# Kernel optimization log

Hardware: AMD Instinct MI355X
Metric: run time of the kernel (lower is better)

## Reference

```python
import jax, jax.numpy as jnp
import numpy as np

T, B, COV, H, L = 512, 256, 128, 512, 2
N_DIST_PARAMS = 2  # lnormal


def setup_inputs() -> dict:
    key = jax.random.key(0)
    ks = jax.random.split(key, 20)
    d = {}
    d["x"] = jax.random.normal(ks[0], (T, B, COV + 1), jnp.float32)
    lengths = jax.random.randint(ks[1], (B,), 2, T + 1)
    lengths = -jnp.sort(-lengths)  # packed sequences: descending lengths
    lengths = lengths.at[0].set(T)  # ensure max length == T
    d["lengths"] = lengths
    d["h0"] = jax.random.normal(ks[2], (L, B, H), jnp.float32)
    s = 1.0 / np.sqrt(H)
    in_dims = [COV + 1, H]
    for l in range(L):
        d[f"Wih{l}"] = jax.random.uniform(ks[3 + 4 * l], (3 * H, in_dims[l]), jnp.float32, -s, s)
        d[f"Whh{l}"] = jax.random.uniform(ks[4 + 4 * l], (3 * H, H), jnp.float32, -s, s)
        d[f"bih{l}"] = jax.random.uniform(ks[5 + 4 * l], (3 * H,), jnp.float32, -s, s)
        d[f"bhh{l}"] = jax.random.uniform(ks[6 + 4 * l], (3 * H,), jnp.float32, -s, s)
    sc = 1.0 / np.sqrt(H + 1)
    d["W_cov"] = jax.random.uniform(ks[11], (COV, H + 1), jnp.float32, -sc, sc)
    d["b_cov"] = jax.random.uniform(ks[12], (COV,), jnp.float32, -sc, sc)
    sp = 1.0 / np.sqrt(L * H)
    d["W_par"] = jax.random.uniform(ks[13], (N_DIST_PARAMS, L * H), jnp.float32, -sp, sp)
    d["b_par"] = jax.random.uniform(ks[14], (N_DIST_PARAMS,), jnp.float32, -sp, sp)
    return d


def gru_layer(x, h0, lengths, Wih, Whh, bih, bhh):
    # x: [T, B, D]; h0: [B, H]. PyTorch GRU gate math, masked for ragged lengths
    gi = jnp.einsum('tbd,gd->tbg', x, Wih) + bih  # [T, B, 3H], one big GEMM
    tt = jnp.arange(x.shape[0])

    def step(h, inp):
        gi_t, t = inp
        gh = h @ Whh.T + bhh
        i_r, i_z, i_n = jnp.split(gi_t, 3, axis=-1)
        h_r, h_z, h_n = jnp.split(gh, 3, axis=-1)
        r = jax.nn.sigmoid(i_r + h_r)
        z = jax.nn.sigmoid(i_z + h_z)
        n = jnp.tanh(i_n + r * h_n)
        h_new = (1.0 - z) * n + z * h
        valid = (t < lengths)[:, None]
        h = jnp.where(valid, h_new, h)          # freeze carry past length
        out = jnp.where(valid, h_new, 0.0)       # pad_packed_sequence zero-pads
        return h, out

    h_last, outs = jax.lax.scan(step, h0, (gi, tt))
    return outs, h_last


def reference(x, lengths, h0, Wih0, Whh0, bih0, bhh0, Wih1, Whh1, bih1, bhh1, W_cov, b_cov, W_par, b_par):
    o0, hl0 = gru_layer(x, h0[0], lengths, Wih0, Whh0, bih0, bhh0)
    o1, hl1 = gru_layer(o0, h0[1], lengths, Wih1, Whh1, bih1, bhh1)
    hs = jnp.transpose(o1, (1, 0, 2))  # [B, T, H]
    times = x[:, :, 0].T               # [B, T]
    hwt = jnp.concatenate([hs, times[..., None]], axis=-1)  # [B, T, H+1]
    Tm = x.shape[0]
    # batched masked matmul replacing per-(batch, timestep) GEMV loop
    preds = jnp.einsum('bth,ch->btc', hwt[:, :Tm - 1], W_cov) + b_cov  # [B, T-1, COV]
    mask = (jnp.arange(Tm - 1)[None, :] < (lengths - 1)[:, None])[..., None]
    preds = jnp.where(mask, preds, 0.0)
    # original writes COV values into a COV+1 wide zero buffer; last channel stays 0
    preds = jnp.concatenate([preds, jnp.zeros(preds.shape[:2] + (1,), preds.dtype)], axis=-1)
    last_hidden = jnp.stack([hl0, hl1])                      # [L, B, H]
    last_flat = jnp.reshape(last_hidden, (last_hidden.shape[1], -1))  # torch .view semantics
    dist_params = last_flat @ W_par.T + b_par
    return preds, jnp.exp(-dist_params)
```

## Files before the change

kernel.cpp:

```cpp
#include <hip/hip_runtime.h>


typedef unsigned short u16;
typedef unsigned long long u64;
typedef __attribute__((ext_vector_type(8))) short short8;
typedef short8 bf16x8;
typedef __attribute__((ext_vector_type(4))) float f32x4;

#define T_DIM 512
#define B_DIM 256
#define H_DIM 512
#define G3H   1536
#define BT    131072
#define XPK   192
#define PRED_ELEMS 16875264
#define SENT  0x7FC0u

#define GLD16(gp, lp) __builtin_amdgcn_global_load_lds( \
    (const __attribute__((address_space(1))) void*)(gp), \
    (__attribute__((address_space(3))) void*)(lp), 16, 0, 0)

__device__ __forceinline__ u16 f2bf(float f) {
    union { float f; unsigned i; } v; v.f = f;
    unsigned i = v.i;
    return (u16)((i + 0x7FFFu + ((i >> 16) & 1u)) >> 16);
}
__device__ __forceinline__ float bf2f(u16 u) {
    union { unsigned i; float f; } v; v.i = ((unsigned)u) << 16; return v.f;
}
__device__ __forceinline__ float sigm(float x) { return 1.f / (1.f + __expf(-x)); }
__device__ __forceinline__ float tanh_f(float x) {
    float ax = fabsf(x);
    float e = __expf(-2.f * ax);
    float t = (1.f - e) / (1.f + e);
    return x < 0.f ? -t : t;
}
__device__ __forceinline__ bf16x8 aload16(const u16* p) {
    union { bf16x8 v; u64 q[2]; } r;
    const u64* qp = (const u64*)p;
    r.q[0] = __hip_atomic_load(qp + 0, __ATOMIC_RELAXED, __HIP_MEMORY_SCOPE_AGENT);
    r.q[1] = __hip_atomic_load(qp + 1, __ATOMIC_RELAXED, __HIP_MEMORY_SCOPE_AGENT);
    return r.v;
}
__device__ __forceinline__ unsigned chk8(bf16x8 v) {
    union { bf16x8 v; unsigned d[4]; } u; u.v = v;
    unsigned b = 0;
#pragma unroll
    for (int i = 0; i < 4; ++i) {
        unsigned d = u.d[i] ^ 0x7FC07FC0u;
        b |= (unsigned)((d & 0xFFFFu) == 0u) | (unsigned)((d >> 16) == 0u);
    }
    return b;
}

__global__ void prep_kernel(const float* __restrict__ Wih0, const float* __restrict__ Wih1,
                            const float* __restrict__ Whh0, const float* __restrict__ Whh1,
                            const float* __restrict__ h0,   const float* __restrict__ Wcov,
                            u16* __restrict__ wih0b, u16* __restrict__ wih1b,
                            u16* __restrict__ whh0b, u16* __restrict__ whh1b,
                            u16* __restrict__ h0bf,  u16* __restrict__ wcovb,
                            float* __restrict__ wlastf,
                            u16* __restrict__ o0c, u16* __restrict__ o1c, int TC) {
    const int gid = blockIdx.x * 256 + threadIdx.x;
    const int gsz = gridDim.x * 256;
    for (int i = gid; i < 128; i += gsz) wlastf[i] = Wcov[i * 513 + 512];
    for (int i = gid; i < 128 * 512; i += gsz) {
        int r = i >> 9, c = i & 511;
        wcovb[i] = f2bf(Wcov[r * 513 + c]);
    }
    for (int i = gid; i < 512 * 512; i += gsz) h0bf[i] = f2bf(h0[i]);
    for (int i = gid; i < 1536 * 192; i += gsz) {
        int r = i / 192, c = i - r * 192;
        wih0b[i] = f2bf(c < 129 ? Wih0[r * 129 + c] : 0.f);
    }
    for (int i = gid; i < 1536 * 512; i += gsz) wih1b[i] = f2bf(Wih1[i]);
    for (int i = gid; i < 1536 * 512; i += gsz) whh0b[i] = f2bf(Whh0[i]);
    for (int i = gid; i < 1536 * 512; i += gsz) whh1b[i] = f2bf(Whh1[i]);
    const u64 SQ = 0x7FC07FC07FC07FC0ULL;
    const size_t nq = (size_t)TC * BT / 4;
    u64* p0 = (u64*)o0c;
    u64* p1 = (u64*)o1c;
    for (size_t i = gid; i < nq; i += gsz) p0[i] = SQ;
    for (size_t i = gid; i < nq; i += gsz) p1[i] = SQ;
}

__global__ void sentinel_kernel(u16* __restrict__ buf, int TC) {
    const u64 SQ = 0x7FC07FC07FC07FC0ULL;
    const size_t nq = (size_t)TC * BT / 4;
    u64* p = (u64*)buf;
    const size_t gid = blockIdx.x * 256 + threadIdx.x;
    const size_t gsz = (size_t)gridDim.x * 256;
    for (size_t i = gid; i < nq; i += gsz) p[i] = SQ;
}

__global__ void cvt_pad_x_kernel(const float* __restrict__ src,
                                 u16* __restrict__ dst, int rows) {
    const int n = rows * 192;
    for (int idx = blockIdx.x * blockDim.x + threadIdx.x; idx < n;
         idx += gridDim.x * blockDim.x) {
        const int row = idx / 192, col = idx - row * 192;
        float v = (col < 129) ? src[(size_t)row * 129 + col] : 0.f;
        dst[idx] = f2bf(v);
    }
}

__global__ __launch_bounds__(256) void gemm_bias_kernel(
    const u16* __restrict__ A, int lda, const u16* __restrict__ B, int ldb,
    const float* __restrict__ bias, u16* __restrict__ C, int ldc, int K) {
    __shared__ __attribute__((aligned(16))) u16 Sh[2][16384];
    const int tid = threadIdx.x, lane = tid & 63, w = tid >> 6;
    const int m0 = blockIdx.y * 128, n0 = blockIdx.x * 128;
    const int r0 = (w & 1) * 64, c0 = (w >> 1) * 64;
    const int am = lane & 15, aq = lane >> 4;
    const int l8 = lane >> 3, lc = lane & 7;
    const int swz = (lc ^ l8) << 3;
    const int NT = K >> 6;
    f32x4 acc[4][4] = {};
#pragma unroll
    for (int s = 0; s < 4; ++s) {
        const int i = w * 4 + s, row = i * 8 + l8;
        GLD16(A + (size_t)(m0 + row) * lda + swz, &Sh[0][i * 512]);
        GLD16(B + (size_t)(n0 + row) * ldb + swz, &Sh[0][8192 + i * 512]);
    }
    __syncthreads();
    int cur = 0;
    for (int kt = 0; kt < NT; ++kt) {
        if (kt + 1 < NT) {
            const int kb = (kt + 1) << 6;
#pragma unroll
            for (int s = 0; s < 4; ++s) {
                const int i = w * 4 + s, row = i * 8 + l8;
                GLD16(A + (size_t)(m0 + row) * lda + kb + swz,
                      &Sh[cur ^ 1][i * 512]);
                GLD16(B + (size_t)(n0 + row) * ldb + kb + swz,
                      &Sh[cur ^ 1][8192 + i * 512]);
            }
        }
        const u16* Ash = &Sh[cur][0];
        const u16* Bsh = &Sh[cur][8192];
#pragma unroll
        for (int ks = 0; ks < 2; ++ks) {
            bf16x8 a[4], bb[4];
#pragma unroll
            for (int f = 0; f < 4; ++f) {
                const int ar = r0 + f * 16 + am;
                a[f] = *(short8*)&Ash[ar * 64 + (((ks * 4 + aq) ^ (ar & 7)) << 3)];
            }
#pragma unroll
            for (int f = 0; f < 4; ++f) {
                const int br = c0 + f * 16 + am;
                bb[f] = *(short8*)&Bsh[br * 64 + (((ks * 4 + aq) ^ (br & 7)) << 3)];
            }
#pragma unroll
            for (int fi = 0; fi < 4; ++fi)
#pragma unroll
                for (int fj = 0; fj < 4; ++fj)
                    acc[fi][fj] = __builtin_amdgcn_mfma_f32_16x16x32_bf16(
                        a[fi], bb[fj], acc[fi][fj], 0, 0, 0);
        }
        __syncthreads();
        cur ^= 1;
    }
    u16* Ep = &Sh[0][0];
#pragma unroll
    for (int fj = 0; fj < 4; ++fj) {
        const int col = c0 + fj * 16 + am;
        const float bia = bias[n0 + col];
#pragma unroll
        for (int fi = 0; fi < 4; ++fi)
#pragma unroll
            for (int r = 0; r < 4; ++r)
                Ep[(r0 + fi * 16 + aq * 4 + r) * 128 + col] =
                    f2bf(acc[fi][fj][r] + bia);
    }
    __syncthreads();
#pragma unroll
    for (int s = 0; s < 8; ++s) {
        const int chunk = tid + s * 256;
        const int row = chunk >> 4, qo = (chunk & 15) * 8;
        *(short8*)(C + (size_t)(m0 + row) * ldc + n0 + qo) =
            *(short8*)&Ep[row * 128 + qo];
    }
}

__global__ __launch_bounds__(256, 2) void scan_gru_kernel(
    const u16* __restrict__ gi,
    const u16* __restrict__ Whh,
    const float* __restrict__ bhh,
    const int* __restrict__ lengths,
    const float* __restrict__ h0l,
    const u16* __restrict__ h0bfl,
    u16* __restrict__ o,
    u16* __restrict__ hcarry,
    float* __restrict__ hlast,
    int t0, int TC) {
    __shared__ __attribute__((aligned(16))) u16 Wl[48 * 520];
    __shared__ __attribute__((aligned(16))) float P[2][12 * 256];
    __shared__ __attribute__((aligned(16))) float bhhf[48];
    const int tid = threadIdx.x, lane = tid & 63, w = tid >> 6;
    const int n0 = blockIdx.x * 16, b0 = blockIdx.y * 16;
#pragma unroll
    for (int it = 0; it < 12; ++it) {
        int f = it * 2048 + tid * 8;
        int j = f >> 9, k = f & 511;
        *(short8*)&Wl[j * 520 + k] =
            *(const short8*)(Whh + ((size_t)((j >> 4) * 512 + n0 + (j & 15))) * 512 + k);
    }
    if (tid < 48) bhhf[tid] = bhh[(tid >> 4) * 512 + n0 + (tid & 15)];
    const int m = tid >> 4, c = tid & 15;
    const int b = b0 + m, col = n0 + c;
    float h = (t0 == 0) ? h0l[(size_t)b * 512 + col]
                        : hlast[(size_t)b * 512 + col];
    const int len = lengths[b];
    const int am = lane & 15, aq = lane >> 4;
    size_t gib = (size_t)b * (size_t)G3H + n0 + c;
    float gr = bf2f(gi[gib]), gz = bf2f(gi[gib + 512]), gn = bf2f(gi[gib + 1024]);
    __syncthreads();
    int pb = 0;
    for (int tl = 0; tl < TC; ++tl) {
        const int t = t0 + tl;
        const u16* Asrc = (tl == 0) ? ((t0 == 0) ? h0bfl : hcarry)
                                    : (o + (size_t)(tl - 1) * BT);
        const u16* arow = Asrc + (size_t)(b0 + am) * 512 + w * 128 + aq * 8;
        bf16x8 av[4];
        if (tl == 0) {
            av[0] = aload16(arow);      av[1] = aload16(arow + 32);
            av[2] = aload16(arow + 64); av[3] = aload16(arow + 96);
        } else {
            for (;;) {
                av[0] = aload16(arow);
                if (!__any((int)chk8(av[0]))) break;
                __builtin_amdgcn_s_sleep(1);
            }
            for (;;) {
                av[1] = aload16(arow + 32);
                av[2] = aload16(arow + 64);
                av[3] = aload16(arow + 96);
                if (!__any((int)(chk8(av[1]) | chk8(av[2]) | chk8(av[3])))) break;
                __builtin_amdgcn_s_sleep(1);
            }
        }
        f32x4 ar = {}, az = {}, an = {};
#pragma unroll
        for (int kb = 0; kb < 4; ++kb) {
            const int k = w * 128 + kb * 32 + aq * 8;
            bf16x8 wr = *(short8*)&Wl[(0 + am) * 520 + k];
            bf16x8 wz = *(short8*)&Wl[(16 + am) * 520 + k];
            bf16x8 wn = *(short8*)&Wl[(32 + am) * 520 + k];
            ar = __builtin_amdgcn_mfma_f32_16x16x32_bf16(av[kb], wr, ar, 0, 0, 0);
            az = __builtin_amdgcn_mfma_f32_16x16x32_bf16(av[kb], wz, az, 0, 0, 0);
            an = __builtin_amdgcn_mfma_f32_16x16x32_bf16(av[kb], wn, an, 0, 0, 0);
        }
#pragma unroll
        for (int r = 0; r < 4; ++r) {
            P[pb][(w * 3 + 0) * 256 + (aq * 4 + r) * 16 + am] = ar[r];
            P[pb][(w * 3 + 1) * 256 + (aq * 4 + r) * 16 + am] = az[r];
            P[pb][(w * 3 + 2) * 256 + (aq * 4 + r) * 16 + am] = an[r];
        }
        __syncthreads();
        float Cr = bhhf[c], Cz = bhhf[16 + c], Cn = bhhf[32 + c];
#pragma unroll
        for (int w2 = 0; w2 < 4; ++w2) {
            Cr += P[pb][(w2 * 3 + 0) * 256 + tid];
            Cz += P[pb][(w2 * 3 + 1) * 256 + tid];
            Cn += P[pb][(w2 * 3 + 2) * 256 + tid];
        }
        float r_ = sigm(gr + Cr);
        float z_ = sigm(gz + Cz);
        float n_ = tanh_f(gn + r_ * Cn);
        float hnew = (1.f - z_) * n_ + z_ * h;
        h = (t < len) ? hnew : h;
        unsigned hb = (unsigned)f2bf(h);
        unsigned part = hb | ((unsigned)__shfl_down((int)hb, 1) << 16);
        unsigned hi2 = (unsigned)__shfl_down((int)part, 2);
        if ((lane & 3) == 0) {
            u64 q = (u64)part | ((u64)hi2 << 32);
            const int mrow = w * 4 + (lane >> 4);
            const int cg = lane & 15;
            __hip_atomic_store(
                (u64*)(o + (size_t)tl * BT + (size_t)(b0 + mrow) * 512 + n0 + cg),
                q, __ATOMIC_RELAXED, __HIP_MEMORY_SCOPE_AGENT);
        }
        if (tl < TC - 1) {
            const size_t gib2 = ((size_t)(tl + 1) * 256 + b) * (size_t)G3H + n0 + c;
            gr = bf2f(gi[gib2]); gz = bf2f(gi[gib2 + 512]); gn = bf2f(gi[gib2 + 1024]);
        } else {
            hcarry[(size_t)b * 512 + col] = f2bf(h);
            hlast[(size_t)b * 512 + col] = h;
        }
        pb ^= 1;
    }
}

__global__ __launch_bounds__(256) void preds_kernel(
    const u16* __restrict__ o1c, const u16* __restrict__ WcovBf,
    const float* __restrict__ wlastf, const float* __restrict__ bcov,
    const float* __restrict__ x, const int* __restrict__ lengths,
    float* __restrict__ out, int t0) {
    __shared__ __attribute__((aligned(16))) u16 Sh[2][16384];
    const int tid = threadIdx.x, lane = tid & 63, w = tid >> 6;
    const int m0 = blockIdx.x * 128;
    const int r0 = (w & 1) * 64, c0 = (w >> 1) * 64;
    const int am = lane & 15, aq = lane >> 4;
    const int l8 = lane >> 3, lc = lane & 7;
    const int swz = (lc ^ l8) << 3;
    f32x4 acc[4][4] = {};
#pragma unroll
    for (int s = 0; s < 4; ++s) {
        const int i = w * 4 + s, row = i * 8 + l8;
        GLD16(o1c + (size_t)(m0 + row) * 512 + swz, &Sh[0][i * 512]);
        GLD16(WcovBf + (size_t)row * 512 + swz, &Sh[0][8192 + i * 512]);
    }
    __syncthreads();
    int cur = 0;
    for (int kt = 0; kt < 8; ++kt) {
        if (kt + 1 < 8) {
            const int kb = (kt + 1) << 6;
#pragma unroll
            for (int s = 0; s < 4; ++s) {
                const int i = w * 4 + s, row = i * 8 + l8;
                GLD16(o1c + (size_t)(m0 + row) * 512 + kb + swz,
                      &Sh[cur ^ 1][i * 512]);
                GLD16(WcovBf + (size_t)row * 512 + kb + swz,
                      &Sh[cur ^ 1][8192 + i * 512]);
            }
        }
        const u16* Ash = &Sh[cur][0];
        const u16* Bsh = &Sh[cur][8192];
#pragma unroll
        for (int ks = 0; ks < 2; ++ks) {
            bf16x8 a[4], bb[4];
#pragma unroll
            for (int f = 0; f < 4; ++f) {
                const int ar2 = r0 + f * 16 + am;
                a[f] = *(short8*)&Ash[ar2 * 64 + (((ks * 4 + aq) ^ (ar2 & 7)) << 3)];
            }
#pragma unroll
            for (int f = 0; f < 4; ++f) {
                const int br = c0 + f * 16 + am;
                bb[f] = *(short8*)&Bsh[br * 64 + (((ks * 4 + aq) ^ (br & 7)) << 3)];
            }
#pragma unroll
            for (int fi = 0; fi < 4; ++fi)
#pragma unroll
                for (int fj = 0; fj < 4; ++fj)
                    acc[fi][fj] = __builtin_amdgcn_mfma_f32_16x16x32_bf16(
                        a[fi], bb[fj], acc[fi][fj], 0, 0, 0);
        }
        __syncthreads();
        cur ^= 1;
    }
    const int tl = m0 >> 8;
    const int t = t0 + tl;
    if (t < 511) {
#pragma unroll
        for (int fj = 0; fj < 4; ++fj) {
            const int cc = c0 + fj * 16 + am;
            const float bc = bcov[cc], wl = wlastf[cc];
#pragma unroll
            for (int fi = 0; fi < 4; ++fi) {
#pragma unroll
                for (int r = 0; r < 4; ++r) {
                    const int row = m0 + r0 + fi * 16 + aq * 4 + r;
                    const int b = row & 255;
                    const bool valid = t < lengths[b] - 1;
                    const float tim = x[(size_t)t * (256 * 129) + b * 129];
                    out[(size_t)b * (511 * 129) + (size_t)t * 129 + cc] =
                        valid ? acc[fi][fj][r] + bc + tim * wl : 0.f;
                }
            }
        }
        if (tid < 128)
            out[(size_t)((m0 & 255) + tid) * (511 * 129) + (size_t)t * 129 + 128] = 0.f;
    }
}

__global__ void dist_kernel(const float* __restrict__ hl0,
                            const float* __restrict__ hl1,
                            const float* __restrict__ Wpar,
                            const float* __restrict__ bpar, float* __restrict__ out) {
    const int w = threadIdx.x >> 6, lane = threadIdx.x & 63;
    const float bp0 = bpar[0], bp1 = bpar[1];
    for (int rr = 0; rr < 8; ++rr) {
        const int i = (blockIdx.x * 4 + w) * 8 + rr;
        const int l = i >> 7, bb = (2 * i) & 255;
        const float* base = (l ? hl1 : hl0) + (size_t)bb * 512;
        float a0 = 0.f, a1 = 0.f;
#pragma unroll
        for (int cc = 0; cc < 16; ++cc) {
            const int k = cc * 64 + lane;
            const float v = base[k];
            a0 += v * Wpar[k];
            a1 += v * Wpar[1024 + k];
        }
#pragma unroll
        for (int off = 32; off; off >>= 1) {
            a0 += __shfl_down(a0, off);
            a1 += __shfl_down(a1, off);
        }
        if (lane == 0) {
            out[PRED_ELEMS + i * 2 + 0] = __expf(-(a0 + bp0));
            out[PRED_ELEMS + i * 2 + 1] = __expf(-(a1 + bp1));
        }
    }
}

extern "C" void kernel_launch(void* const* d_in, const int* in_sizes, int n_in,
                              void* d_out, int out_size, void* d_ws, size_t ws_size,
                              hipStream_t stream) {
    const float* x    = (const float*)d_in[0];
    const int* lens   = (const int*)d_in[1];
    const float* h0   = (const float*)d_in[2];
    const float* Wih0 = (const float*)d_in[3];
    const float* Whh0 = (const float*)d_in[4];
    const float* bih0 = (const float*)d_in[5];
    const float* bhh0 = (const float*)d_in[6];
    const float* Wih1 = (const float*)d_in[7];
    const float* Whh1 = (const float*)d_in[8];
    const float* bih1 = (const float*)d_in[9];
    const float* bhh1 = (const float*)d_in[10];
    const float* Wcov = (const float*)d_in[11];
    const float* bcov = (const float*)d_in[12];
    const float* Wpar = (const float*)d_in[13];
    const float* bpar = (const float*)d_in[14];
    float* out = (float*)d_out;
    char* wsb = (char*)d_ws;

    size_t off = 0;
    auto take = [&](size_t bytes) -> size_t {
        size_t r = off; off += (bytes + 255) & ~(size_t)255; return r;
    };
    const size_t oHl0   = take((size_t)BT * 4);
    const size_t oHl1   = take((size_t)BT * 4);
    const size_t oHc0   = take((size_t)BT * 2);
    const size_t oHc1   = take((size_t)BT * 2);
    const size_t oH0bf  = take((size_t)2 * BT * 2);
    const size_t oWih0b = take((size_t)G3H * XPK * 2);
    const size_t oWih1b = take((size_t)G3H * 512 * 2);
    const size_t oWhh0b = take((size_t)G3H * 512 * 2);
    const size_t oWhh1b = take((size_t)G3H * 512 * 2);
    const size_t oWcovb = take((size_t)128 * 512 * 2);
    const size_t oWlast = take(512);
    const size_t fixed = off;

    const size_t per = (size_t)256 * XPK * 2 + (size_t)256 * G3H * 2 +
                       2 * (size_t)256 * 512 * 2 + 2048;
    const size_t remain = ws_size > fixed ? ws_size - fixed : 0;
    int TC = 1;
    const int cands[10] = {512, 256, 128, 64, 32, 16, 8, 4, 2, 1};
    for (int i = 0; i < 10; ++i)
        if ((size_t)cands[i] * per <= remain) { TC = cands[i]; break; }

    const size_t oXbf = take((size_t)TC * 256 * XPK * 2);
    const size_t oGi  = take((size_t)TC * 256 * G3H * 2);
    const size_t oO0  = take((size_t)TC * 256 * 512 * 2);
    const size_t oO1  = take((size_t)TC * 256 * 512 * 2);

    float* hl0  = (float*)(wsb + oHl0);
    float* hl1  = (float*)(wsb + oHl1);
    u16* hcar0  = (u16*)(wsb + oHc0);
    u16* hcar1  = (u16*)(wsb + oHc1);
    u16* h0bf   = (u16*)(wsb + oH0bf);
    u16* wih0b  = (u16*)(wsb + oWih0b);
    u16* wih1b  = (u16*)(wsb + oWih1b);
    u16* whh0b  = (u16*)(wsb + oWhh0b);
    u16* whh1b  = (u16*)(wsb + oWhh1b);
    u16* wcovb  = (u16*)(wsb + oWcovb);
    float* wlastf = (float*)(wsb + oWlast);
    u16* xbfc   = (u16*)(wsb + oXbf);
    u16* gic    = (u16*)(wsb + oGi);
    u16* o0c    = (u16*)(wsb + oO0);
    u16* o1c    = (u16*)(wsb + oO1);

    prep_kernel<<<1024, 256, 0, stream>>>(Wih0, Wih1, Whh0, Whh1, h0, Wcov,
                                          wih0b, wih1b, whh0b, whh1b, h0bf,
                                          wcovb, wlastf, o0c, o1c, TC);

    for (int t0 = 0; t0 < T_DIM; t0 += TC) {
        int n = TC * 256 * XPK;
        int pg = (n + 255) / 256; if (pg > 2048) pg = 2048;
        cvt_pad_x_kernel<<<pg, 256, 0, stream>>>(
            x + (size_t)t0 * 256 * 129, xbfc, TC * 256);
        gemm_bias_kernel<<<dim3(12, TC * 2), 256, 0, stream>>>(
            xbfc, XPK, wih0b, XPK, bih0, gic, G3H, XPK);
        if (t0 > 0)
            sentinel_kernel<<<2048, 256, 0, stream>>>(o0c, TC);
        scan_gru_kernel<<<dim3(32, 16), 256, 0, stream>>>(
            gic, whh0b, bhh0, lens, h0, h0bf, o0c, hcar0, hl0, t0, TC);
        gemm_bias_kernel<<<dim3(12, TC * 2), 256, 0, stream>>>(
            o0c, H_DIM, wih1b, H_DIM, bih1, gic, G3H, H_DIM);
        if (t0 > 0)
            sentinel_kernel<<<2048, 256, 0, stream>>>(o1c, TC);
        scan_gru_kernel<<<dim3(32, 16), 256, 0, stream>>>(
            gic, whh1b, bhh1, lens, h0 + (size_t)BT, h0bf + (size_t)BT,
            o1c, hcar1, hl1, t0, TC);
        preds_kernel<<<dim3(TC * 2), 256, 0, stream>>>(
            o1c, wcovb, wlastf, bcov, x, lens, out, t0);
    }
    dist_kernel<<<8, 256, 0, stream>>>(hl0, hl1, Wpar, bpar, out);
}
```

Before: 4.531 ms.

## Fuse input-projection GEMM into the recurrent GRU scan kernel

```diff
diff --git a/kernel.cpp b/kernel.cpp
--- a/kernel.cpp
+++ b/kernel.cpp
@@ -12,9 +12,8 @@
 #define H_DIM 512
 #define G3H   1536
 #define BT    131072
-#define XPK   192
+#define XPK   256
 #define PRED_ELEMS 16875264
-#define SENT  0x7FC0u
 
 #define GLD16(gp, lp) __builtin_amdgcn_global_load_lds( \
     (const __attribute__((address_space(1))) void*)(gp), \
@@ -69,8 +68,8 @@
         wcovb[i] = f2bf(Wcov[r * 513 + c]);
     }
     for (int i = gid; i < 512 * 512; i += gsz) h0bf[i] = f2bf(h0[i]);
-    for (int i = gid; i < 1536 * 192; i += gsz) {
-        int r = i / 192, c = i - r * 192;
+    for (int i = gid; i < 1536 * XPK; i += gsz) {
+        int r = i >> 8, c = i & 255;
         wih0b[i] = f2bf(c < 129 ? Wih0[r * 129 + c] : 0.f);
     }
     for (int i = gid; i < 1536 * 512; i += gsz) wih1b[i] = f2bf(Wih1[i]);
@@ -95,96 +94,20 @@
 
 __global__ void cvt_pad_x_kernel(const float* __restrict__ src,
                                  u16* __restrict__ dst, int rows) {
-    const int n = rows * 192;
+    const int n = rows * 256;
     for (int idx = blockIdx.x * blockDim.x + threadIdx.x; idx < n;
          idx += gridDim.x * blockDim.x) {
-        const int row = idx / 192, col = idx - row * 192;
+        const int row = idx >> 8, col = idx & 255;
         float v = (col < 129) ? src[(size_t)row * 129 + col] : 0.f;
         dst[idx] = f2bf(v);
     }
 }
 
-__global__ __launch_bounds__(256) void gemm_bias_kernel(
-    const u16* __restrict__ A, int lda, const u16* __restrict__ B, int ldb,
-    const float* __restrict__ bias, u16* __restrict__ C, int ldc, int K) {
-    __shared__ __attribute__((aligned(16))) u16 Sh[2][16384];
-    const int tid = threadIdx.x, lane = tid & 63, w = tid >> 6;
-    const int m0 = blockIdx.y * 128, n0 = blockIdx.x * 128;
-    const int r0 = (w & 1) * 64, c0 = (w >> 1) * 64;
-    const int am = lane & 15, aq = lane >> 4;
-    const int l8 = lane >> 3, lc = lane & 7;
-    const int swz = (lc ^ l8) << 3;
-    const int NT = K >> 6;
-    f32x4 acc[4][4] = {};
-#pragma unroll
-    for (int s = 0; s < 4; ++s) {
-        const int i = w * 4 + s, row = i * 8 + l8;
-        GLD16(A + (size_t)(m0 + row) * lda + swz, &Sh[0][i * 512]);
-        GLD16(B + (size_t)(n0 + row) * ldb + swz, &Sh[0][8192 + i * 512]);
-    }
-    __syncthreads();
-    int cur = 0;
-    for (int kt = 0; kt < NT; ++kt) {
-        if (kt + 1 < NT) {
-            const int kb = (kt + 1) << 6;
-#pragma unroll
-            for (int s = 0; s < 4; ++s) {
-                const int i = w * 4 + s, row = i * 8 + l8;
-                GLD16(A + (size_t)(m0 + row) * lda + kb + swz,
-                      &Sh[cur ^ 1][i * 512]);
-                GLD16(B + (size_t)(n0 + row) * ldb + kb + swz,
-                      &Sh[cur ^ 1][8192 + i * 512]);
-            }
-        }
-        const u16* Ash = &Sh[cur][0];
-        const u16* Bsh = &Sh[cur][8192];
-#pragma unroll
-        for (int ks = 0; ks < 2; ++ks) {
-            bf16x8 a[4], bb[4];
-#pragma unroll
-            for (int f = 0; f < 4; ++f) {
-                const int ar = r0 + f * 16 + am;
-                a[f] = *(short8*)&Ash[ar * 64 + (((ks * 4 + aq) ^ (ar & 7)) << 3)];
-            }
-#pragma unroll
-            for (int f = 0; f < 4; ++f) {
-                const int br = c0 + f * 16 + am;
-                bb[f] = *(short8*)&Bsh[br * 64 + (((ks * 4 + aq) ^ (br & 7)) << 3)];
-            }
-#pragma unroll
-            for (int fi = 0; fi < 4; ++fi)
-#pragma unroll
-                for (int fj = 0; fj < 4; ++fj)
-                    acc[fi][fj] = __builtin_amdgcn_mfma_f32_16x16x32_bf16(
-                        a[fi], bb[fj], acc[fi][fj], 0, 0, 0);
-        }
-        __syncthreads();
-        cur ^= 1;
-    }
-    u16* Ep = &Sh[0][0];
-#pragma unroll
-    for (int fj = 0; fj < 4; ++fj) {
-        const int col = c0 + fj * 16 + am;
-        const float bia = bias[n0 + col];
-#pragma unroll
-        for (int fi = 0; fi < 4; ++fi)
-#pragma unroll
-            for (int r = 0; r < 4; ++r)
-                Ep[(r0 + fi * 16 + aq * 4 + r) * 128 + col] =
-                    f2bf(acc[fi][fj][r] + bia);
-    }
-    __syncthreads();
-#pragma unroll
-    for (int s = 0; s < 8; ++s) {
-        const int chunk = tid + s * 256;
-        const int row = chunk >> 4, qo = (chunk & 15) * 8;
-        *(short8*)(C + (size_t)(m0 + row) * ldc + n0 + qo) =
-            *(short8*)&Ep[row * 128 + qo];
-    }
-}
-
-__global__ __launch_bounds__(256, 2) void scan_gru_kernel(
-    const u16* __restrict__ gi,
+template<int AK>
+__global__ __launch_bounds__(256, 2) void scan_fused_kernel(
+    const u16* __restrict__ xin,
+    const u16* __restrict__ Wih,
+    const float* __restrict__ bih,
     const u16* __restrict__ Whh,
     const float* __restrict__ bhh,
     const int* __restrict__ lengths,
@@ -195,10 +118,13 @@
     float* __restrict__ hlast,
     int t0, int TC) {
     __shared__ __attribute__((aligned(16))) u16 Wl[48 * 520];
-    __shared__ __attribute__((aligned(16))) float P[2][12 * 256];
-    __shared__ __attribute__((aligned(16))) float bhhf[48];
+    __shared__ __attribute__((aligned(16))) float P[16 * 256];
+    __shared__ __attribute__((aligned(16))) float bRZ[32], bNX[16], bNH[16];
     const int tid = threadIdx.x, lane = tid & 63, w = tid >> 6;
     const int n0 = blockIdx.x * 16, b0 = blockIdx.y * 16;
+    const int am = lane & 15, aq = lane >> 4;
+    constexpr int KW = AK / 4;
+    constexpr int KB2 = KW / 32;
 #pragma unroll
     for (int it = 0; it < 12; ++it) {
         int f = it * 2048 + tid * 8;
@@ -206,19 +132,36 @@
         *(short8*)&Wl[j * 520 + k] =
             *(const short8*)(Whh + ((size_t)((j >> 4) * 512 + n0 + (j & 15))) * 512 + k);
     }
-    if (tid < 48) bhhf[tid] = bhh[(tid >> 4) * 512 + n0 + (tid & 15)];
+    if (tid < 32) bRZ[tid] = bih[(tid >> 4) * 512 + n0 + (tid & 15)] +
+                             bhh[(tid >> 4) * 512 + n0 + (tid & 15)];
+    else if (tid < 48) bNX[tid - 32] = bih[1024 + n0 + (tid - 32)];
+    else if (tid < 64) bNH[tid - 48] = bhh[1024 + n0 + (tid - 48)];
+    bf16x8 wf[3][KB2];
+#pragma unroll
+    for (int g = 0; g < 3; ++g)
+#pragma unroll
+        for (int kb = 0; kb < KB2; ++kb)
+            wf[g][kb] = *(const short8*)(Wih +
+                (size_t)(g * 512 + n0 + am) * AK + w * KW + kb * 32 + aq * 8);
     const int m = tid >> 4, c = tid & 15;
     const int b = b0 + m, col = n0 + c;
     float h = (t0 == 0) ? h0l[(size_t)b * 512 + col]
                         : hlast[(size_t)b * 512 + col];
     const int len = lengths[b];
-    const int am = lane & 15, aq = lane >> 4;
-    size_t gib = (size_t)b * (size_t)G3H + n0 + c;
-    float gr = bf2f(gi[gib]), gz = bf2f(gi[gib + 512]), gn = bf2f(gi[gib + 1024]);
+    bf16x8 xa[KB2];
+#pragma unroll
+    for (int kb = 0; kb < KB2; ++kb)
+        xa[kb] = *(const short8*)(xin + (size_t)(b0 + am) * AK + w * KW + kb * 32 + aq * 8);
     __syncthreads();
-    int pb = 0;
     for (int tl = 0; tl < TC; ++tl) {
         const int t = t0 + tl;
+        f32x4 ar = {}, az = {}, anx = {}, anh = {};
+#pragma unroll
+        for (int kb = 0; kb < KB2; ++kb) {
+            ar  = __builtin_amdgcn_mfma_f32_16x16x32_bf16(xa[kb], wf[0][kb], ar, 0, 0, 0);
+            az  = __builtin_amdgcn_mfma_f32_16x16x32_bf16(xa[kb], wf[1][kb], az, 0, 0, 0);
+            anx = __builtin_amdgcn_mfma_f32_16x16x32_bf16(xa[kb], wf[2][kb], anx, 0, 0, 0);
+        }
         const u16* Asrc = (tl == 0) ? ((t0 == 0) ? h0bfl : hcarry)
                                     : (o + (size_t)(tl - 1) * BT);
         const u16* arow = Asrc + (size_t)(b0 + am) * 512 + w * 128 + aq * 8;
@@ -240,34 +183,36 @@
                 __builtin_amdgcn_s_sleep(1);
             }
         }
-        f32x4 ar = {}, az = {}, an = {};
 #pragma unroll
         for (int kb = 0; kb < 4; ++kb) {
             const int k = w * 128 + kb * 32 + aq * 8;
             bf16x8 wr = *(short8*)&Wl[(0 + am) * 520 + k];
             bf16x8 wz = *(short8*)&Wl[(16 + am) * 520 + k];
             bf16x8 wn = *(short8*)&Wl[(32 + am) * 520 + k];
-            ar = __builtin_amdgcn_mfma_f32_16x16x32_bf16(av[kb], wr, ar, 0, 0, 0);
-            az = __builtin_amdgcn_mfma_f32_16x16x32_bf16(av[kb], wz, az, 0, 0, 0);
-            an = __builtin_amdgcn_mfma_f32_16x16x32_bf16(av[kb], wn, an, 0, 0, 0);
+            ar  = __builtin_amdgcn_mfma_f32_16x16x32_bf16(av[kb], wr, ar, 0, 0, 0);
+            az  = __builtin_amdgcn_mfma_f32_16x16x32_bf16(av[kb], wz, az, 0, 0, 0);
+            anh = __builtin_amdgcn_mfma_f32_16x16x32_bf16(av[kb], wn, anh, 0, 0, 0);
         }
 #pragma unroll
         for (int r = 0; r < 4; ++r) {
-            P[pb][(w * 3 + 0) * 256 + (aq * 4 + r) * 16 + am] = ar[r];
-            P[pb][(w * 3 + 1) * 256 + (aq * 4 + r) * 16 + am] = az[r];
-            P[pb][(w * 3 + 2) * 256 + (aq * 4 + r) * 16 + am] = an[r];
+            P[(w * 4 + 0) * 256 + (aq * 4 + r) * 16 + am] = ar[r];
+            P[(w * 4 + 1) * 256 + (aq * 4 + r) * 16 + am] = az[r];
+            P[(w * 4 + 2) * 256 + (aq * 4 + r) * 16 + am] = anx[r];
+            P[(w * 4 + 3) * 256 + (aq * 4 + r) * 16 + am] = anh[r];
         }
         __syncthreads();
-        float Cr = bhhf[c], Cz = bhhf[16 + c], Cn = bhhf[32 + c];
+        float Cr = bRZ[c], Cz = bRZ[16 + c], Nx = bNX[c], Nh = bNH[c];
 #pragma unroll
         for (int w2 = 0; w2 < 4; ++w2) {
-            Cr += P[pb][(w2 * 3 + 0) * 256 + tid];
-            Cz += P[pb][(w2 * 3 + 1) * 256 + tid];
-            Cn += P[pb][(w2 * 3 + 2) * 256 + tid];
-        }
-        float r_ = sigm(gr + Cr);
-        float z_ = sigm(gz + Cz);
-        float n_ = tanh_f(gn + r_ * Cn);
+            Cr += P[(w2 * 4 + 0) * 256 + tid];
+            Cz += P[(w2 * 4 + 1) * 256 + tid];
+            Nx += P[(w2 * 4 + 2) * 256 + tid];
+            Nh += P[(w2 * 4 + 3) * 256 + tid];
+        }
+        __syncthreads();
+        float r_ = sigm(Cr);
+        float z_ = sigm(Cz);
+        float n_ = tanh_f(Nx + r_ * Nh);
         float hnew = (1.f - z_) * n_ + z_ * h;
         h = (t < len) ? hnew : h;
         unsigned hb = (unsigned)f2bf(h);
@@ -282,13 +227,14 @@
                 q, __ATOMIC_RELAXED, __HIP_MEMORY_SCOPE_AGENT);
         }
         if (tl < TC - 1) {
-            const size_t gib2 = ((size_t)(tl + 1) * 256 + b) * (size_t)G3H + n0 + c;
-            gr = bf2f(gi[gib2]); gz = bf2f(gi[gib2 + 512]); gn = bf2f(gi[gib2 + 1024]);
+#pragma unroll
+            for (int kb = 0; kb < KB2; ++kb)
+                xa[kb] = *(const short8*)(xin +
+                    ((size_t)(tl + 1) * 256 + b0 + am) * AK + w * KW + kb * 32 + aq * 8);
         } else {
             hcarry[(size_t)b * 512 + col] = f2bf(h);
             hlast[(size_t)b * 512 + col] = h;
         }
-        pb ^= 1;
     }
 }
 
@@ -443,7 +389,7 @@
     const size_t oWlast = take(512);
     const size_t fixed = off;
 
-    const size_t per = (size_t)256 * XPK * 2 + (size_t)256 * G3H * 2 +
+    const size_t per = (size_t)256 * XPK * 2 +
                        2 * (size_t)256 * 512 * 2 + 2048;
     const size_t remain = ws_size > fixed ? ws_size - fixed : 0;
     int TC = 1;
@@ -452,7 +398,6 @@
         if ((size_t)cands[i] * per <= remain) { TC = cands[i]; break; }
 
     const size_t oXbf = take((size_t)TC * 256 * XPK * 2);
-    const size_t oGi  = take((size_t)TC * 256 * G3H * 2);
     const size_t oO0  = take((size_t)TC * 256 * 512 * 2);
     const size_t oO1  = take((size_t)TC * 256 * 512 * 2);
 
@@ -468,7 +413,6 @@
     u16* wcovb  = (u16*)(wsb + oWcovb);
     float* wlastf = (float*)(wsb + oWlast);
     u16* xbfc   = (u16*)(wsb + oXbf);
-    u16* gic    = (u16*)(wsb + oGi);
     u16* o0c    = (u16*)(wsb + oO0);
     u16* o1c    = (u16*)(wsb + oO1);
 
@@ -481,19 +425,16 @@
         int pg = (n + 255) / 256; if (pg > 2048) pg = 2048;
         cvt_pad_x_kernel<<<pg, 256, 0, stream>>>(
             x + (size_t)t0 * 256 * 129, xbfc, TC * 256);
-        gemm_bias_kernel<<<dim3(12, TC * 2), 256, 0, stream>>>(
-            xbfc, XPK, wih0b, XPK, bih0, gic, G3H, XPK);
         if (t0 > 0)
             sentinel_kernel<<<2048, 256, 0, stream>>>(o0c, TC);
-        scan_gru_kernel<<<dim3(32, 16), 256, 0, stream>>>(
-            gic, whh0b, bhh0, lens, h0, h0bf, o0c, hcar0, hl0, t0, TC);
-        gemm_bias_kernel<<<dim3(12, TC * 2), 256, 0, stream>>>(
-            o0c, H_DIM, wih1b, H_DIM, bih1, gic, G3H, H_DIM);
+        scan_fused_kernel<XPK><<<dim3(32, 16), 256, 0, stream>>>(
+            xbfc, wih0b, bih0, whh0b, bhh0, lens, h0, h0bf,
+            o0c, hcar0, hl0, t0, TC);
         if (t0 > 0)
             sentinel_kernel<<<2048, 256, 0, stream>>>(o1c, TC);
-        scan_gru_kernel<<<dim3(32, 16), 256, 0, stream>>>(
-            gic, whh1b, bhh1, lens, h0 + (size_t)BT, h0bf + (size_t)BT,
-            o1c, hcar1, hl1, t0, TC);
+        scan_fused_kernel<512><<<dim3(32, 16), 256, 0, stream>>>(
+            o0c, wih1b, bih1, whh1b, bhh1, lens, h0 + (size_t)BT,
+            h0bf + (size_t)BT, o1c, hcar1, hl1, t0, TC);
         preds_kernel<<<dim3(TC * 2), 256, 0, stream>>>(
             o1c, wcovb, wlastf, bcov, x, lens, out, t0);
     }
```

After: 4.047 ms. 10.7% less time.
